# Performance work log

Hardware: AMD Instinct MI355X
Metric: run time of the kernel (lower is better)

## Reference

```python
import jax, jax.numpy as jnp
import numpy as np

NEG_SLOPE = 0.01  # torch nn.LeakyReLU default


def leaky_relu(x):
    return jnp.where(x >= 0, x, NEG_SLOPE * x)


def sc_layer(Ld, Lu, x, P, Q):
    # Ld, Lu: [N, N, K]; x: [N, F_in]; P, Q: [F_in, F_out, K]
    # Equivalent to sum_k Ld[:,:,k] @ x @ P[:,:,k]  (+ Lu analog).
    # Contract small feature dim first, then one pass over the big stacks.
    xp = jnp.einsum('mf,fgk->mgk', x, P)  # [N, F_out, K] (tiny)
    xq = jnp.einsum('mf,fgk->mgk', x, Q)
    return jnp.einsum('nmk,mgk->ng', Ld, xp) + jnp.einsum('nmk,mgk->ng', Lu, xq)


def setup_inputs() -> dict:
    key = jax.random.key(0)
    ks = jax.random.split(key, 9)
    N, K, L = 4096, 5, 3
    v = 0.01
    return {
        'LdStack': jax.random.normal(ks[0], (N, N, K), dtype=jnp.float32),
        'LuStack': jax.random.normal(ks[1], (N, N, K), dtype=jnp.float32),
        'x': jax.random.normal(ks[2], (N, 1), dtype=jnp.float32),
        'P1': v * jax.random.normal(ks[3], (1, L, K), dtype=jnp.float32),
        'Q1': v * jax.random.normal(ks[4], (1, L, K), dtype=jnp.float32),
        'P2': v * jax.random.normal(ks[5], (L, L, K), dtype=jnp.float32),
        'Q2': v * jax.random.normal(ks[6], (L, L, K), dtype=jnp.float32),
        'P3': v * jax.random.normal(ks[7], (L, 1, K), dtype=jnp.float32),
        'Q3': v * jax.random.normal(ks[8], (L, 1, K), dtype=jnp.float32),
    }


def reference(LdStack, LuStack, x, P1, Q1, P2, Q2, P3, Q3):
    h1 = sc_layer(LdStack, LuStack, x, P1, Q1)                 # [N, L]
    h2 = sc_layer(LdStack, LuStack, leaky_relu(h1), P2, Q2)    # [N, L]
    h3 = sc_layer(LdStack, LuStack, leaky_relu(h2), P3, Q3)    # [N, 1]
    return h3
```

## Files before the change

### kernel.cpp

```cpp
#include <hip/hip_runtime.h>

#define NTHREADS 256
#define KDIM 5
#define CHUNK_M 256
#define CHUNK_FLOATS (CHUNK_M * KDIM)
#define NCHUNK (4096 / CHUNK_M)

typedef float __attribute__((address_space(3))) lds_f;
typedef const float __attribute__((address_space(1))) glb_f;

template <int FIN, int FOUT, bool ACT>
__global__ __launch_bounds__(NTHREADS)
void sc_pass(const float* __restrict__ Ld, const float* __restrict__ Lu,
             const float* __restrict__ v,
             const float* __restrict__ P,
             const float* __restrict__ Q,
             float* __restrict__ out)
{
    constexpr int N = 4096;
    constexpr int NA = KDIM * FIN;

    __shared__ float lds[2][2][CHUNK_FLOATS];
    __shared__ float red[NTHREADS / 64][2 * NA];

    const int n    = blockIdx.x;
    const int tid  = threadIdx.x;
    const int wid  = tid >> 6;
    const int lane = tid & 63;

    const float* __restrict__ ldrow = Ld + (size_t)n * N * KDIM;
    const float* __restrict__ lurow = Lu + (size_t)n * N * KDIM;

    auto stage = [&](int c, int b) {
#pragma unroll
        for (int i = 0; i < 5; ++i) {
            const int off = c * CHUNK_FLOATS + i * 256 + wid * 64 + lane;
            __builtin_amdgcn_global_load_lds((glb_f*)(ldrow + off),
                                             (lds_f*)&lds[b][0][i * 256 + wid * 64],
                                             4, 0, 0);
        }
#pragma unroll
        for (int i = 0; i < 5; ++i) {
            const int off = c * CHUNK_FLOATS + i * 256 + wid * 64 + lane;
            __builtin_amdgcn_global_load_lds((glb_f*)(lurow + off),
                                             (lds_f*)&lds[b][1][i * 256 + wid * 64],
                                             4, 0, 0);
        }
    };

    float accd[NA], accu[NA];
#pragma unroll
    for (int j = 0; j < NA; ++j) { accd[j] = 0.f; accu[j] = 0.f; }

    stage(0, 0);
    stage(1, 1);

    for (int c = 0; c < NCHUNK; ++c) {
        if (c + 1 < NCHUNK) asm volatile("s_waitcnt vmcnt(10)" ::: "memory");
        else                asm volatile("s_waitcnt vmcnt(0)"  ::: "memory");
        __builtin_amdgcn_s_barrier();

        const int b = c & 1;
        const int m = c * CHUNK_M + tid;

        float sv[FIN];
#pragma unroll
        for (int f = 0; f < FIN; ++f) sv[f] = v[(size_t)m * FIN + f];

        float ldv[KDIM], luv[KDIM];
#pragma unroll
        for (int q = 0; q < KDIM; ++q) {
            ldv[q] = lds[b][0][tid * KDIM + q];
            luv[q] = lds[b][1][tid * KDIM + q];
        }
#pragma unroll
        for (int k = 0; k < KDIM; ++k)
#pragma unroll
            for (int f = 0; f < FIN; ++f) {
                accd[k * FIN + f] += ldv[k] * sv[f];
                accu[k * FIN + f] += luv[k] * sv[f];
            }

        asm volatile("" ::: "memory");
        __builtin_amdgcn_s_barrier();
        if (c + 2 < NCHUNK) stage(c + 2, b);
    }

#pragma unroll
    for (int j = 0; j < NA; ++j) {
        float vd = accd[j], vu = accu[j];
#pragma unroll
        for (int off = 32; off > 0; off >>= 1) {
            vd += __shfl_xor(vd, off);
            vu += __shfl_xor(vu, off);
        }
        if (lane == 0) { red[wid][j] = vd; red[wid][NA + j] = vu; }
    }
    __syncthreads();

    if (tid == 0) {
        float h[FOUT];
#pragma unroll
        for (int g = 0; g < FOUT; ++g) h[g] = 0.f;
#pragma unroll
        for (int k = 0; k < KDIM; ++k)
#pragma unroll
            for (int f = 0; f < FIN; ++f) {
                float td = 0.f, tu = 0.f;
#pragma unroll
                for (int w = 0; w < NTHREADS / 64; ++w) {
                    td += red[w][k * FIN + f];
                    tu += red[w][NA + k * FIN + f];
                }
#pragma unroll
                for (int g = 0; g < FOUT; ++g) {
                    h[g] += td * P[(f * FOUT + g) * KDIM + k]
                          + tu * Q[(f * FOUT + g) * KDIM + k];
                }
            }
#pragma unroll
        for (int g = 0; g < FOUT; ++g) {
            float hv = h[g];
            out[(size_t)n * FOUT + g] = ACT ? (hv >= 0.f ? hv : 0.01f * hv) : hv;
        }
    }
}

extern "C" void kernel_launch(void* const* d_in, const int* in_sizes, int n_in,
                              void* d_out, int out_size, void* d_ws, size_t ws_size,
                              hipStream_t stream) {
    constexpr int N = 4096;
    const float* Ld = (const float*)d_in[0];
    const float* Lu = (const float*)d_in[1];
    const float* x  = (const float*)d_in[2];
    const float* P1 = (const float*)d_in[3];
    const float* Q1 = (const float*)d_in[4];
    const float* P2 = (const float*)d_in[5];
    const float* Q2 = (const float*)d_in[6];
    const float* P3 = (const float*)d_in[7];
    const float* Q3 = (const float*)d_in[8];
    float* out = (float*)d_out;

    float* s1 = (float*)d_ws;
    float* s2 = s1 + (size_t)N * 3;

    sc_pass<1, 3, true ><<<N, NTHREADS, 0, stream>>>(Ld, Lu, x,  P1, Q1, s1);
    sc_pass<3, 3, true ><<<N, NTHREADS, 0, stream>>>(Ld, Lu, s1, P2, Q2, s2);
    sc_pass<3, 1, false><<<N, NTHREADS, 0, stream>>>(Ld, Lu, s2, P3, Q3, out);
}
```

Before: 357.9 us.

## Deepen LDS pipeline to four buffers with 16-byte async loads and staged v

Raises the async global-to-LDS ring from two to four buffers with three chunks in flight. It issues the next stage right after the barrier, so the second barrier per iteration goes away. Most Ld/Lu staging switches to 16-byte global_load_lds, which cuts the instruction count. The activation vector v is also prefetched into LDS instead of read straight from global memory. The cost is more LDS per block, which may lower occupancy, and hand-tuned vmcnt thresholds that must match the exact number of issued loads.

After: 392.6 us. 9.7% more time.

```diff
diff --git a/kernel.cpp b/kernel.cpp
--- a/kernel.cpp
+++ b/kernel.cpp
@@ -5,6 +5,9 @@
 #define CHUNK_M 256
 #define CHUNK_FLOATS (CHUNK_M * KDIM)
 #define NCHUNK (4096 / CHUNK_M)
+#define NBUF 4
+
+#define WAITV(n) asm volatile("s_waitcnt vmcnt(" #n ")" ::: "memory")
 
 typedef float __attribute__((address_space(3))) lds_f;
 typedef const float __attribute__((address_space(1))) glb_f;
@@ -19,8 +22,11 @@
 {
     constexpr int N = 4096;
     constexpr int NA = KDIM * FIN;
+    constexpr int VCHUNK = CHUNK_M * FIN;
 
-    __shared__ float lds[2][2][CHUNK_FLOATS];
+    __shared__ float sLd[NBUF][CHUNK_FLOATS];
+    __shared__ float sLu[NBUF][CHUNK_FLOATS];
+    __shared__ float sV [NBUF][VCHUNK];
     __shared__ float red[NTHREADS / 64][2 * NA];
 
     const int n    = blockIdx.x;
@@ -32,19 +38,22 @@
     const float* __restrict__ lurow = Lu + (size_t)n * N * KDIM;
 
     auto stage = [&](int c, int b) {
+        const size_t cbase = (size_t)c * CHUNK_FLOATS;
+        const int wf = wid * 320;
+        __builtin_amdgcn_global_load_lds((glb_f*)(ldrow + cbase + wf + lane * 4),
+                                         (lds_f*)&sLd[b][wf], 16, 0, 0);
+        __builtin_amdgcn_global_load_lds((glb_f*)(ldrow + cbase + wf + 256 + lane),
+                                         (lds_f*)&sLd[b][wf + 256], 4, 0, 0);
+        __builtin_amdgcn_global_load_lds((glb_f*)(lurow + cbase + wf + lane * 4),
+                                         (lds_f*)&sLu[b][wf], 16, 0, 0);
+        __builtin_amdgcn_global_load_lds((glb_f*)(lurow + cbase + wf + 256 + lane),
+                                         (lds_f*)&sLu[b][wf + 256], 4, 0, 0);
+        const int vf = wid * 64 * FIN;
 #pragma unroll
-        for (int i = 0; i < 5; ++i) {
-            const int off = c * CHUNK_FLOATS + i * 256 + wid * 64 + lane;
-            __builtin_amdgcn_global_load_lds((glb_f*)(ldrow + off),
-                                             (lds_f*)&lds[b][0][i * 256 + wid * 64],
-                                             4, 0, 0);
-        }
-#pragma unroll
-        for (int i = 0; i < 5; ++i) {
-            const int off = c * CHUNK_FLOATS + i * 256 + wid * 64 + lane;
-            __builtin_amdgcn_global_load_lds((glb_f*)(lurow + off),
-                                             (lds_f*)&lds[b][1][i * 256 + wid * 64],
-                                             4, 0, 0);
+        for (int j = 0; j < FIN; ++j) {
+            __builtin_amdgcn_global_load_lds(
+                (glb_f*)(v + (size_t)c * VCHUNK + vf + j * 64 + lane),
+                (lds_f*)&sV[b][vf + j * 64], 4, 0, 0);
         }
     };
 
@@ -54,24 +63,33 @@
 
     stage(0, 0);
     stage(1, 1);
+    stage(2, 2);
 
     for (int c = 0; c < NCHUNK; ++c) {
-        if (c + 1 < NCHUNK) asm volatile("s_waitcnt vmcnt(10)" ::: "memory");
-        else                asm volatile("s_waitcnt vmcnt(0)"  ::: "memory");
+        const int R = NCHUNK - c;
+        if constexpr (FIN == 3) {
+            if (R > 2)       WAITV(14);
+            else if (R == 2) WAITV(7);
+            else             WAITV(0);
+        } else {
+            if (R > 2)       WAITV(10);
+            else if (R == 2) WAITV(5);
+            else             WAITV(0);
+        }
         __builtin_amdgcn_s_barrier();
+        if (c + 3 < NCHUNK) stage(c + 3, (c + 3) & 3);
 
-        const int b = c & 1;
-        const int m = c * CHUNK_M + tid;
+        const int b = c & 3;
 
         float sv[FIN];
 #pragma unroll
-        for (int f = 0; f < FIN; ++f) sv[f] = v[(size_t)m * FIN + f];
+        for (int f = 0; f < FIN; ++f) sv[f] = sV[b][tid * FIN + f];
 
         float ldv[KDIM], luv[KDIM];
 #pragma unroll
         for (int q = 0; q < KDIM; ++q) {
-            ldv[q] = lds[b][0][tid * KDIM + q];
-            luv[q] = lds[b][1][tid * KDIM + q];
+            ldv[q] = sLd[b][tid * KDIM + q];
+            luv[q] = sLu[b][tid * KDIM + q];
         }
 #pragma unroll
         for (int k = 0; k < KDIM; ++k)
@@ -82,8 +100,6 @@
             }
 
         asm volatile("" ::: "memory");
-        __builtin_amdgcn_s_barrier();
-        if (c + 2 < NCHUNK) stage(c + 2, b);
     }
 
 #pragma unroll
```

## Replace LDS double-buffered async staging with direct strided global loads

Applied to the files above, without the earlier changes.

Removes the global_load_lds double-buffered pipeline and its barriers, and instead has each thread load its five Ld and five Lu values straight from global memory. The launch bounds now request 8 blocks per CU so more waves can hide latency. The cost is uncoalesced 20-byte-strided accesses per thread, relying on the cache to merge them. It also gives up explicit prefetch depth.

New measurement: 426.7 us. 1.19x slower.

```diff
diff --git a/kernel.cpp b/kernel.cpp
--- a/kernel.cpp
+++ b/kernel.cpp
@@ -2,15 +2,9 @@
 
 #define NTHREADS 256
 #define KDIM 5
-#define CHUNK_M 256
-#define CHUNK_FLOATS (CHUNK_M * KDIM)
-#define NCHUNK (4096 / CHUNK_M)
-
-typedef float __attribute__((address_space(3))) lds_f;
-typedef const float __attribute__((address_space(1))) glb_f;
 
 template <int FIN, int FOUT, bool ACT>
-__global__ __launch_bounds__(NTHREADS)
+__global__ __launch_bounds__(NTHREADS, 8)
 void sc_pass(const float* __restrict__ Ld, const float* __restrict__ Lu,
              const float* __restrict__ v,
              const float* __restrict__ P,
@@ -19,9 +13,7 @@
 {
     constexpr int N = 4096;
     constexpr int NA = KDIM * FIN;
-
-    __shared__ float lds[2][2][CHUNK_FLOATS];
-    __shared__ float red[NTHREADS / 64][2 * NA];
+    constexpr int NITER = N / NTHREADS;
 
     const int n    = blockIdx.x;
     const int tid  = threadIdx.x;
@@ -31,48 +23,23 @@
     const float* __restrict__ ldrow = Ld + (size_t)n * N * KDIM;
     const float* __restrict__ lurow = Lu + (size_t)n * N * KDIM;
 
-    auto stage = [&](int c, int b) {
-#pragma unroll
-        for (int i = 0; i < 5; ++i) {
-            const int off = c * CHUNK_FLOATS + i * 256 + wid * 64 + lane;
-            __builtin_amdgcn_global_load_lds((glb_f*)(ldrow + off),
-                                             (lds_f*)&lds[b][0][i * 256 + wid * 64],
-                                             4, 0, 0);
-        }
-#pragma unroll
-        for (int i = 0; i < 5; ++i) {
-            const int off = c * CHUNK_FLOATS + i * 256 + wid * 64 + lane;
-            __builtin_amdgcn_global_load_lds((glb_f*)(lurow + off),
-                                             (lds_f*)&lds[b][1][i * 256 + wid * 64],
-                                             4, 0, 0);
-        }
-    };
-
     float accd[NA], accu[NA];
 #pragma unroll
     for (int j = 0; j < NA; ++j) { accd[j] = 0.f; accu[j] = 0.f; }
 
-    stage(0, 0);
-    stage(1, 1);
+    for (int i = 0; i < NITER; ++i) {
+        const int m = i * NTHREADS + tid;
+        const float* __restrict__ pd = ldrow + (size_t)m * KDIM;
+        const float* __restrict__ pu = lurow + (size_t)m * KDIM;
 
-    for (int c = 0; c < NCHUNK; ++c) {
-        if (c + 1 < NCHUNK) asm volatile("s_waitcnt vmcnt(10)" ::: "memory");
-        else                asm volatile("s_waitcnt vmcnt(0)"  ::: "memory");
-        __builtin_amdgcn_s_barrier();
-
-        const int b = c & 1;
-        const int m = c * CHUNK_M + tid;
-
-        float sv[FIN];
+        float ldv[KDIM], luv[KDIM], sv[FIN];
+#pragma unroll
+        for (int q = 0; q < KDIM; ++q) ldv[q] = pd[q];
+#pragma unroll
+        for (int q = 0; q < KDIM; ++q) luv[q] = pu[q];
 #pragma unroll
         for (int f = 0; f < FIN; ++f) sv[f] = v[(size_t)m * FIN + f];
 
-        float ldv[KDIM], luv[KDIM];
-#pragma unroll
-        for (int q = 0; q < KDIM; ++q) {
-            ldv[q] = lds[b][0][tid * KDIM + q];
-            luv[q] = lds[b][1][tid * KDIM + q];
-        }
 #pragma unroll
         for (int k = 0; k < KDIM; ++k)
 #pragma unroll
@@ -80,12 +47,9 @@
                 accd[k * FIN + f] += ldv[k] * sv[f];
                 accu[k * FIN + f] += luv[k] * sv[f];
             }
-
-        asm volatile("" ::: "memory");
-        __builtin_amdgcn_s_barrier();
-        if (c + 2 < NCHUNK) stage(c + 2, b);
     }
 
+    __shared__ float red[NTHREADS / 64][2 * NA];
 #pragma unroll
     for (int j = 0; j < NA; ++j) {
         float vd = accd[j], vu = accu[j];
```
